# Kernel optimization log

Hardware: AMD Instinct MI355X
Metric: run time of the kernel (lower is better)

## Reference

```python
import jax, jax.numpy as jnp
import numpy as np

WINDOW, STRIDE, BLUR_THR, EPS = 8, 4, 50.0, 1e-5
DN = ('NCHW', 'OIHW', 'NCHW')


def _conv(x, w, pad=0, stride=1):
    return jax.lax.conv_general_dilated(x, w, (stride, stride), [(pad, pad), (pad, pad)], dimension_numbers=DN)


def _detect_rgb_invalid(rgb):
    # Laplacian-variance blur detector: unfold(8,stride=4) -> var -> threshold -> scatter windows
    B, _, H, W = rgb.shape
    gray = 0.299 * rgb[:, 0] + 0.587 * rgb[:, 1] + 0.114 * rgb[:, 2]
    gray = jnp.clip(gray * 255.0, 0.0, 255.0)[:, None]  # [B,1,H,W]
    lap_k = jnp.array([[0., 1., 0.], [1., -4., 1.], [0., 1., 0.]], gray.dtype)[None, None]
    lap = _conv(gray, lap_k, pad=1)
    ones_k = jnp.ones((1, 1, WINDOW, WINDOW), gray.dtype)
    s1 = jax.lax.conv_general_dilated(lap, ones_k, (STRIDE, STRIDE), 'VALID', dimension_numbers=DN)
    s2 = jax.lax.conv_general_dilated(lap * lap, ones_k, (STRIDE, STRIDE), 'VALID', dimension_numbers=DN)
    n = float(WINDOW * WINDOW)
    var = (s2 - s1 * s1 / n) / (n - 1.0)  # unbiased var, matches torch.var
    flags = (var[:, 0] < BLUR_THR).astype(gray.dtype)  # [B, hs, ws]
    hs, ws = flags.shape[1], flags.shape[2]
    rep = jnp.repeat(jnp.repeat(flags, STRIDE, axis=1), STRIDE, axis=2)  # [B, hs*4, ws*4]
    mask = jnp.zeros((B, H, W), gray.dtype)
    # each 8x8 window covers 2x2 stride-cells -> max over the 4 shifted copies
    for dy in range(0, WINDOW, STRIDE):
        for dx in range(0, WINDOW, STRIDE):
            mask = mask.at[:, dy:dy + hs * STRIDE, dx:dx + ws * STRIDE].max(rep)
    return mask


def _bn_relu(x, g, b):
    m = x.mean((0, 2, 3), keepdims=True)
    v = x.var((0, 2, 3), keepdims=True)  # biased, matches BN training-mode normalization
    return jax.nn.relu(g[None, :, None, None] * (x - m) / jnp.sqrt(v + EPS) + b[None, :, None, None])


def _attend(main, aux, inv, ft_w, bn_g, bn_b, sa_w, ca1_w, ca2_w):
    B, C, H, W = main.shape
    aux_t = _bn_relu(_conv(aux, ft_w, pad=1), bn_g, bn_b)
    xs = jnp.broadcast_to(jnp.linspace(-1.0, 1.0, W, dtype=main.dtype)[None, None, None, :], (B, 1, H, W))
    ys = jnp.broadcast_to(jnp.linspace(-1.0, 1.0, H, dtype=main.dtype)[None, None, :, None], (B, 1, H, W))
    sp_in = jnp.concatenate([main.mean(1, keepdims=True), main.max(axis=1, keepdims=True), xs, ys], axis=1)
    sw = jax.nn.sigmoid(_conv(sp_in, sa_w, pad=3))  # [B,1,H,W]
    gap = main.mean((2, 3), keepdims=True)
    cw = jax.nn.sigmoid(_conv(jax.nn.relu(_conv(gap, ca1_w)), ca2_w))  # [B,C,1,1]
    return aux_t * sw * cw * (1.0 + inv[:, None])


def _compensate(main, aux, inv, params):
    # early-return when mask is all-zero in torch is mathematically identical to the blend
    comp = _attend(main, aux, inv, *params)
    m = inv[:, None]
    return main * (1.0 - m) + comp * m


def _down(mask, h, w):
    H, W = mask.shape[1], mask.shape[2]
    return mask[:, ::H // h, ::W // w]  # exact nearest-neighbor for integer ratios


def _forward(rgb_feat0, rgb_feat1, rgb_feat2, depth_feat0, depth_feat1, depth_feat2, rgb_img, depth_img,
             ft_w0, bn_g0, bn_b0, sa_w0, ca1_w0, ca2_w0,
             ft_w1, bn_g1, bn_b1, sa_w1, ca1_w1, ca2_w1,
             ft_w2, bn_g2, bn_b2, sa_w2, ca1_w2, ca2_w2):
    rgb_mask = _detect_rgb_invalid(rgb_img)
    depth_mask = (depth_img[:, 2] <= 0.0).astype(rgb_img.dtype)
    rgb_feats = (rgb_feat0, rgb_feat1, rgb_feat2)
    depth_feats = (depth_feat0, depth_feat1, depth_feat2)
    params = ((ft_w0, bn_g0, bn_b0, sa_w0, ca1_w0, ca2_w0),
              (ft_w1, bn_g1, bn_b1, sa_w1, ca1_w1, ca2_w1),
              (ft_w2, bn_g2, bn_b2, sa_w2, ca1_w2, ca2_w2))
    outs_r, outs_d = [], []
    for rf, df, p in zip(rgb_feats, depth_feats, params):
        h, w = rf.shape[2], rf.shape[3]
        ri = _down(rgb_mask, h, w)
        di = _down(depth_mask, h, w)
        outs_r.append(_compensate(rf, df, ri, p))
        outs_d.append(_compensate(df, rf, di, p))
    return tuple(outs_r) + tuple(outs_d)


def setup_inputs() -> dict:
    key = jax.random.key(0)
    ks = iter(jax.random.split(key, 40))
    B, H, W = 8, 512, 512
    chans = [256, 512, 1024]
    feat_hw = [(64, 64), (32, 32), (16, 16)]
    d = {}
    for i, (C, (fh, fw)) in enumerate(zip(chans, feat_hw)):
        d[f'rgb_feat{i}'] = jax.random.normal(next(ks), (B, C, fh, fw), jnp.float32)
        d[f'depth_feat{i}'] = jax.random.normal(next(ks), (B, C, fh, fw), jnp.float32)
    d['rgb_img'] = jax.random.uniform(next(ks), (B, 3, H, W), jnp.float32)
    d['depth_img'] = jax.random.normal(next(ks), (B, 3, H, W), jnp.float32)
    for i, C in enumerate(chans):
        r = C // 16
        d[f'ft_w{i}'] = jax.random.normal(next(ks), (C, C, 3, 3), jnp.float32) * 0.02
        d[f'bn_g{i}'] = jnp.ones((C,), jnp.float32)
        d[f'bn_b{i}'] = jnp.zeros((C,), jnp.float32)
        d[f'sa_w{i}'] = jax.random.normal(next(ks), (1, 4, 7, 7), jnp.float32) * 0.1
        d[f'ca1_w{i}'] = jax.random.normal(next(ks), (r, C, 1, 1), jnp.float32) * 0.1
        d[f'ca2_w{i}'] = jax.random.normal(next(ks), (C, r, 1, 1), jnp.float32) * 0.1
    return d


def reference(rgb_feat0, rgb_feat1, rgb_feat2, depth_feat0, depth_feat1, depth_feat2, rgb_img, depth_img,
              ft_w0, bn_g0, bn_b0, sa_w0, ca1_w0, ca2_w0,
              ft_w1, bn_g1, bn_b1, sa_w1, ca1_w1, ca2_w1,
              ft_w2, bn_g2, bn_b2, sa_w2, ca1_w2, ca2_w2):
    return _forward(rgb_feat0, rgb_feat1, rgb_feat2, depth_feat0, depth_feat1, depth_feat2, rgb_img, depth_img,
                    ft_w0, bn_g0, bn_b0, sa_w0, ca1_w0, ca2_w0,
                    ft_w1, bn_g1, bn_b1, sa_w1, ca1_w1, ca2_w1,
                    ft_w2, bn_g2, bn_b2, sa_w2, ca1_w2, ca2_w2)
```

## Files before the change

kernel.cpp:

```cpp
#include <hip/hip_runtime.h>
#include <math.h>

#define B8 8
typedef unsigned short ushort_t;
typedef __attribute__((ext_vector_type(8))) short bf16x8;
typedef __attribute__((ext_vector_type(4))) float f32x4;

static __device__ __forceinline__ float sigmoidf_(float x){ return 1.f/(1.f+expf(-x)); }

static __device__ __forceinline__ ushort_t f2bf(float f){
  unsigned u = __float_as_uint(f);
  u = u + 0x7fffu + ((u>>16)&1u);
  return (ushort_t)(u>>16);
}
static __device__ __forceinline__ float bflo(unsigned q){ return __uint_as_float(q << 16); }
static __device__ __forceinline__ float bfhi(unsigned q){ return __uint_as_float(q & 0xffff0000u); }

__device__ __forceinline__ void gload_lds16(const ushort_t* g, ushort_t* l){
  __builtin_amdgcn_global_load_lds((const __attribute__((address_space(1))) unsigned int*)(const void*)g,
                                   (__attribute__((address_space(3))) unsigned int*)(void*)l, 16, 0, 0);
}

__global__ __launch_bounds__(256) void k_flags2(const float* __restrict__ rgb,
                                                float* __restrict__ flags){
  __shared__ float sg[70][71];
  int bx = blockIdx.x & 7, by = (blockIdx.x >> 3) & 7, b = blockIdx.x >> 6;
  int wy0 = by*16, wx0 = bx*16;
  int y0 = 4*wy0 - 1, x0 = 4*wx0 - 1;
  const float* p = rgb + (size_t)b*3*262144;
  int tid = threadIdx.x;
  for (int i = tid; i < 70*70; i += 256){
    int r = i/70, cX = i%70;
    int y = y0 + r, x = x0 + cX;
    float v = 0.f;
    if (y>=0 && y<512 && x>=0 && x<512){
      int ii = y*512+x;
      v = 0.299f*p[ii] + 0.587f*p[ii+262144] + 0.114f*p[ii+524288];
      v = fminf(fmaxf(v*255.f, 0.f), 255.f);
    }
    sg[r][cX] = v;
  }
  __syncthreads();
  int wy = wy0 + (tid>>4), wx = wx0 + (tid&15);
  if (wy > 126 || wx > 126) return;
  int ry = 4*(tid>>4) + 1, rx = 4*(tid&15) + 1;
  float s1 = 0.f, s2 = 0.f;
  #pragma unroll
  for (int iy=0; iy<8; ++iy){
    int r = ry+iy;
    #pragma unroll
    for (int ix=0; ix<8; ++ix){
      int cX = rx+ix;
      float c = sg[r][cX];
      float lap = sg[r-1][cX] + sg[r+1][cX] + sg[r][cX-1] + sg[r][cX+1] - 4.f*c;
      s1 += lap; s2 += lap*lap;
    }
  }
  float var = (s2 - s1*s1*(1.f/64.f)) * (1.f/63.f);
  flags[(size_t)b*16129 + wy*127 + wx] = (var < 50.f) ? 1.f : 0.f;
}

__global__ void k_masks3(const float* __restrict__ flags, const float* __restrict__ depth,
                         float* __restrict__ ri0, float* __restrict__ di0,
                         float* __restrict__ ri1, float* __restrict__ di1,
                         float* __restrict__ ri2, float* __restrict__ di2){
  int idx = blockIdx.x*256 + threadIdx.x;
  const int n0 = 8*4096, n1 = 8*1024, n2 = 8*256;
  float* ri; float* di; int h, st, i2;
  if (idx < n0){ ri=ri0; di=di0; h=64; st=8;  i2=idx; }
  else if (idx < n0+n1){ ri=ri1; di=di1; h=32; st=16; i2=idx-n0; }
  else if (idx < n0+n1+n2){ ri=ri2; di=di2; h=16; st=32; i2=idx-n0-n1; }
  else return;
  int b = i2/(h*h), i = i2%(h*h);
  int y = (i/h)*st, x = (i%h)*st;
  const float* f = flags + (size_t)b*16129;
  int fy = y>>2, fx = x>>2;
  float v = f[fy*127+fx];
  if (y>0)         v = fmaxf(v, f[(fy-1)*127+fx]);
  if (x>0)         v = fmaxf(v, f[fy*127+fx-1]);
  if (y>0 && x>0)  v = fmaxf(v, f[(fy-1)*127+fx-1]);
  ri[i2] = v;
  const int IHW = 262144;
  di[i2] = (depth[(size_t)b*3*IHW + 2*IHW + (size_t)y*512 + x] <= 0.f) ? 1.f : 0.f;
}

template<int C>
__global__ __launch_bounds__(256) void k_wrd2(const float* __restrict__ w, ushort_t* __restrict__ outp){
  __shared__ float swp[9*C];
  int co = blockIdx.x, tid = threadIdx.x;
  const int n = 9*C;
  const float* src = w + (size_t)co*n;
  for (int i=tid;i<n;i+=256) swp[i]=src[i];
  __syncthreads();
  ushort_t* dst = outp + (size_t)co*n;
  for (int j=tid;j<n;j+=256){
    int cb  = j / 576;
    int rem = j - cb*576;
    int kq  = rem >> 6;
    int cin = rem & 63;
    dst[j] = f2bf(swp[(cb*64 + cin)*9 + kq]);
  }
}

template<int C, int H, int W>
__global__ __launch_bounds__(256) void k_nhwc2(const float* __restrict__ rgbf,
                                               const float* __restrict__ depf,
                                               ushort_t* __restrict__ outp){
  const int W2 = W+2, H2 = H+2, CB = C/64;
  const int NHSZ = B8*H2*W2*C;
  __shared__ float st[64*66];
  int bi = blockIdx.x;
  int dir = bi & 1; bi >>= 1;
  int cb  = bi % CB; bi /= CB;
  int yy  = bi % H2;
  int b   = bi / H2;
  int tid = threadIdx.x;
  const float* in = (dir==0) ? depf : rgbf;
  ushort_t* outrow = outp + (size_t)dir*NHSZ + ((size_t)(b*H2 + yy)*W2)*C + cb*64;
  bool pad_row = (yy == 0) || (yy == H2-1);
  if (!pad_row){
    int y = yy-1;
    const float* src = in + ((size_t)(b*C + cb*64)*H + y)*W;
    for (int i=tid; i<64*W; i+=256){
      int c = i / W, x = i % W;
      st[x*66 + c] = src[(size_t)c*H*W + x];
    }
  }
  __syncthreads();
  for (int j=tid; j<W2*8; j+=256){
    int x = j >> 3, cc = (j & 7)*8;
    ushort_t tmp[8];
    if (pad_row || x == 0 || x == W2-1){
      #pragma unroll
      for (int q=0;q<8;++q) tmp[q]=0;
    } else {
      const float* sp = &st[(x-1)*66 + cc];
      float2 a0 = *(const float2*)(sp+0);
      float2 a1 = *(const float2*)(sp+2);
      float2 a2 = *(const float2*)(sp+4);
      float2 a3 = *(const float2*)(sp+6);
      tmp[0]=f2bf(a0.x); tmp[1]=f2bf(a0.y); tmp[2]=f2bf(a1.x); tmp[3]=f2bf(a1.y);
      tmp[4]=f2bf(a2.x); tmp[5]=f2bf(a2.y); tmp[6]=f2bf(a3.x); tmp[7]=f2bf(a3.y);
    }
    *(bf16x8*)&outrow[(size_t)x*C + cc] = *(bf16x8*)tmp;
  }
}

template<int C, int H, int W, int KS>
__global__ __launch_bounds__(512)
void k_gemm_conv(const ushort_t* __restrict__ Aw, const ushort_t* __restrict__ nh,
                 ushort_t* __restrict__ Gm){
  const int K9 = 9*C;
  const int HW = H*W;
  const int N  = B8*HW;
  const int H2 = H+2, W2 = W+2;
  const int NT_N = N/256, NT_M = C/256;
  const int KCT = 36;
  const int NHSZ = B8*H2*W2*C;
  __shared__ ushort_t sA[2][16384];
  __shared__ ushort_t sB[2][16384];
  int tid = threadIdx.x;

  const int nwg = 2*KS*NT_M*NT_N;
  const int MK  = 2*KS*NT_M;
  int bid = blockIdx.x;
  int swz = (bid & 7)*(nwg >> 3) + (bid >> 3);
  int mk  = swz % MK;
  int n_t = swz / MK;
  int m_t = mk % NT_M;
  int kz2 = mk / NT_M;
  int dir = kz2 / KS, kz = kz2 % KS;

  const ushort_t* nhd = nh + (size_t)dir*NHSZ;
  int m0 = m_t*256, n0 = n_t*256;
  int l = tid & 63, wv_id = tid >> 6;
  int wm = wv_id >> 2, wn = wv_id & 3;
  int lrow = l & 15, lq = l >> 4;
  int lx7 = lrow & 7;

  long long aoffA[2][2], boffB[2][2];
  #pragma unroll
  for (int h=0; h<2; ++h){
    #pragma unroll
    for (int j=0; j<2; ++j){
      int c = j*512 + tid;
      int lr = h*128 + (c>>3);
      int slot = c & 7;
      int lslot = slot ^ (lr & 7);
      int q_ = lr >> 6, wm_ = (lr>>5)&1, loc = lr & 31;
      int r = wm_*128 + q_*32 + loc;
      aoffA[h][j] = (long long)(m0 + r)*K9 + lslot*8;
      int nn = n0 + lr;
      int b_ = nn / HW, rhw = nn % HW;
      int y = rhw / W, x = rhw % W;
      boffB[h][j] = ((long long)(b_*H2 + y + 1)*W2 + (x + 1))*(long long)C + lslot*8;
    }
  }

#define STAGE_A(s_, h_, kc_) do{                                    \
    long long oK = (long long)(kc_) << 6;                           \
    ushort_t* d0 = &sA[s_][(h_)*8192 + tid*8];                      \
    gload_lds16(Aw + aoffA[h_][0] + oK, d0);                        \
    gload_lds16(Aw + aoffA[h_][1] + oK, d0 + 4096);                 \
  }while(0)
#define STAGE_B(s_, h_, kc_) do{                                    \
    int cb_ = (kc_)/9, kq_ = (kc_) - cb_*9;                         \
    long long dv = (long long)((kq_/3 - 1)*W2 + (kq_%3 - 1))*C + ((long long)cb_<<6); \
    ushort_t* d0 = &sB[s_][(h_)*8192 + tid*8];                      \
    gload_lds16(nhd + boffB[h_][0] + dv, d0);                       \
    gload_lds16(nhd + boffB[h_][1] + dv, d0 + 4096);                \
  }while(0)

  f32x4 acc[8][4];
  #pragma unroll
  for (int i=0;i<8;++i)
    #pragma unroll
    for (int j=0;j<4;++j) acc[i][j] = (f32x4){0.f,0.f,0.f,0.f};

  int kc0 = kz*KCT;

  STAGE_A(0,0,kc0);   STAGE_A(0,1,kc0);
  STAGE_B(0,0,kc0);   STAGE_B(0,1,kc0);
  STAGE_B(1,0,kc0+1); STAGE_B(1,1,kc0+1);
  STAGE_A(1,0,kc0+1);
  asm volatile("s_waitcnt vmcnt(6)" ::: "memory");
  __builtin_amdgcn_s_barrier();

  for (int t=0; t<KCT; ++t){
    int cur = t & 1, nxt = cur ^ 1;
    int kc = kc0 + t;
    bf16x8 bf[4][2], afA[2][2], afB[2][2];

    #pragma unroll
    for (int ni=0;ni<4;++ni)
      #pragma unroll
      for (int kk=0;kk<2;++kk)
        bf[ni][kk] = *(const bf16x8*)&sB[cur][(wn*64 + ni*16 + lrow)*64 + ((kk*4+lq)^lx7)*8];
    #pragma unroll
    for (int mi=0;mi<2;++mi)
      #pragma unroll
      for (int kk=0;kk<2;++kk)
        afA[mi][kk] = *(const bf16x8*)&sA[cur][(wm*32 + mi*16 + lrow)*64 + ((kk*4+lq)^lx7)*8];
    #pragma unroll
    for (int mi=0;mi<2;++mi)
      #pragma unroll
      for (int kk=0;kk<2;++kk)
        afB[mi][kk] = *(const bf16x8*)&sA[cur][(64 + wm*32 + mi*16 + lrow)*64 + ((kk*4+lq)^lx7)*8];
    if (t+1 < KCT) STAGE_A(nxt,1,kc+1);
    __builtin_amdgcn_s_setprio(1);
    #pragma unroll
    for (int kk=0;kk<2;++kk)
      #pragma unroll
      for (int mi=0;mi<2;++mi)
        #pragma unroll
        for (int ni=0;ni<4;++ni)
          acc[mi][ni] = __builtin_amdgcn_mfma_f32_16x16x32_bf16(afA[mi][kk], bf[ni][kk], acc[mi][ni], 0,0,0);
    __builtin_amdgcn_s_setprio(0);
    asm volatile("s_waitcnt lgkmcnt(0)" ::: "memory");
    __builtin_amdgcn_sched_barrier(0);
    __builtin_amdgcn_s_barrier();

    #pragma unroll
    for (int mi=0;mi<2;++mi)
      #pragma unroll
      for (int kk=0;kk<2;++kk)
        afA[mi][kk] = *(const bf16x8*)&sA[cur][(128 + wm*32 + mi*16 + lrow)*64 + ((kk*4+lq)^lx7)*8];
    if (t+2 < KCT) STAGE_B(cur,0,kc+2);
    __builtin_amdgcn_s_setprio(1);
    #pragma unroll
    for (int kk=0;kk<2;++kk)
      #pragma unroll
      for (int mi=0;mi<2;++mi)
        #pragma unroll
        for (int ni=0;ni<4;++ni)
          acc[2+mi][ni] = __builtin_amdgcn_mfma_f32_16x16x32_bf16(afB[mi][kk], bf[ni][kk], acc[2+mi][ni], 0,0,0);
    __builtin_amdgcn_s_setprio(0);

    #pragma unroll
    for (int mi=0;mi<2;++mi)
      #pragma unroll
      for (int kk=0;kk<2;++kk)
        afB[mi][kk] = *(const bf16x8*)&sA[cur][(192 + wm*32 + mi*16 + lrow)*64 + ((kk*4+lq)^lx7)*8];
    if (t+2 < KCT) STAGE_B(cur,1,kc+2);
    __builtin_amdgcn_s_setprio(1);
    #pragma unroll
    for (int kk=0;kk<2;++kk)
      #pragma unroll
      for (int mi=0;mi<2;++mi)
        #pragma unroll
        for (int ni=0;ni<4;++ni)
          acc[4+mi][ni] = __builtin_amdgcn_mfma_f32_16x16x32_bf16(afA[mi][kk], bf[ni][kk], acc[4+mi][ni], 0,0,0);
    __builtin_amdgcn_s_setprio(0);

    if (t+2 < KCT) STAGE_A(cur,0,kc+2);
    __builtin_amdgcn_s_setprio(1);
    #pragma unroll
    for (int kk=0;kk<2;++kk)
      #pragma unroll
      for (int mi=0;mi<2;++mi)
        #pragma unroll
        for (int ni=0;ni<4;++ni)
          acc[6+mi][ni] = __builtin_amdgcn_mfma_f32_16x16x32_bf16(afB[mi][kk], bf[ni][kk], acc[6+mi][ni], 0,0,0);
    __builtin_amdgcn_s_setprio(0);
    if (t+2 < KCT) { asm volatile("s_waitcnt vmcnt(6)" ::: "memory"); }
    else           { asm volatile("s_waitcnt vmcnt(0)" ::: "memory"); }
    __builtin_amdgcn_sched_barrier(0);
    __builtin_amdgcn_s_barrier();
  }
#undef STAGE_A
#undef STAGE_B

  ushort_t* po = Gm + (size_t)kz2*C*N;
  #pragma unroll
  for (int ai=0;ai<8;++ai)
    #pragma unroll
    for (int ni=0;ni<4;++ni)
      #pragma unroll
      for (int r=0;r<4;++r)
        po[(size_t)(m0 + wm*128 + ai*16 + lq*4 + r)*N + n0 + wn*64 + ni*16 + lrow] = f2bf(acc[ai][ni][r]);
}

template<int C, int HW, int SPLIT>
__global__ __launch_bounds__(256) void k_sg(const float* __restrict__ rgbf,
                                            const float* __restrict__ depf,
                                            float* __restrict__ gpart,
                                            float* __restrict__ pmean,
                                            float* __restrict__ pmax_){
  const int CG = C/32;
  const int POS = HW/SPLIT;
  int dir = blockIdx.y;
  const float* main_ = (dir==0) ? rgbf : depf;
  int bi = blockIdx.x;
  int sp = bi % SPLIT; bi /= SPLIT;
  int cg = bi % CG;    int b = bi / CG;
  const float* base = main_ + ((size_t)b*C + (size_t)cg*32)*HW + (size_t)sp*POS;
  int tid = threadIdx.x;
  float csum[32];
  #pragma unroll
  for (int c=0;c<32;++c) csum[c]=0.f;
  size_t po = ((size_t)dir*CG + cg)*((size_t)B8*HW) + (size_t)b*HW + (size_t)sp*POS;

  if constexpr (POS >= 1024){
    const int P4 = POS/4;
    for (int p = tid; p < P4; p += 256){
      float4 ps = {0.f,0.f,0.f,0.f};
      float4 pm = {-INFINITY,-INFINITY,-INFINITY,-INFINITY};
      #pragma unroll
      for (int c=0;c<32;++c){
        float4 v = *(const float4*)(base + (size_t)c*HW + (size_t)p*4);
        csum[c] += v.x+v.y+v.z+v.w;
        ps.x+=v.x; ps.y+=v.y; ps.z+=v.z; ps.w+=v.w;
        pm.x=fmaxf(pm.x,v.x); pm.y=fmaxf(pm.y,v.y); pm.z=fmaxf(pm.z,v.z); pm.w=fmaxf(pm.w,v.w);
      }
      *(float4*)(pmean + po + (size_t)p*4) = ps;
      *(float4*)(pmax_ + po + (size_t)p*4) = pm;
    }
  } else {
    int p = tid;
    if (p < POS){
      float ps = 0.f, pm = -INFINITY;
      #pragma unroll
      for (int c=0;c<32;++c){
        float v = base[(size_t)c*HW + p];
        csum[c] += v;
        ps += v; pm = fmaxf(pm, v);
      }
      pmean[po + p] = ps;
      pmax_[po + p] = pm;
    }
  }
  __shared__ float red[4][32];
  int lane = tid & 63, w = tid >> 6;
  #pragma unroll
  for (int c=0;c<32;++c){
    float s = csum[c];
    #pragma unroll
    for (int off=32; off; off>>=1) s += __shfl_down(s, off);
    if (lane == 0) red[w][c] = s;
  }
  __syncthreads();
  if (tid < 32){
    float s = red[0][tid]+red[1][tid]+red[2][tid]+red[3][tid];
    gpart[(((size_t)dir*B8 + b)*SPLIT + sp)*C + (size_t)cg*32 + tid] = s;
  }
}

__global__ void k_sgc(const float* __restrict__ pmean, const float* __restrict__ pmax_,
                      float* __restrict__ spmean, float* __restrict__ spmax,
                      int CG, int BHW, float invC){
  int dir = blockIdx.y;
  int p = blockIdx.x*256 + threadIdx.x;
  if (p >= BHW) return;
  const float* pm = pmean + (size_t)dir*CG*BHW;
  const float* px = pmax_ + (size_t)dir*CG*BHW;
  float s = 0.f, m = -INFINITY;
  for (int g=0; g<CG; ++g){
    s += pm[(size_t)g*BHW + p];
    m = fmaxf(m, px[(size_t)g*BHW + p]);
  }
  spmean[(size_t)dir*BHW + p] = s*invC;
  spmax [(size_t)dir*BHW + p] = m;
}

__global__ void k_sw(const float* __restrict__ spmean, const float* __restrict__ spmax,
                     const float* __restrict__ sa, float* __restrict__ sw,
                     int H, int W){
  __shared__ float s_sa[196];
  int tid = threadIdx.x;
  if (tid < 196) s_sa[tid] = sa[tid];
  __syncthreads();
  int HW = H*W;
  int dir = blockIdx.y;
  int gpos = blockIdx.x*256 + tid;
  if (gpos >= B8*HW) return;
  int b = gpos/HW, i = gpos%HW;
  int y = i/W, x = i%W;
  float inv_w = 2.f/(float)(W-1), inv_h = 2.f/(float)(H-1);
  const float* pm = spmean + (size_t)dir*B8*HW + (size_t)b*HW;
  const float* px = spmax  + (size_t)dir*B8*HW + (size_t)b*HW;
  float acc = 0.f;
  for (int ky=0;ky<7;++ky){
    int yy = y+ky-3;
    if (yy<0 || yy>=H) continue;
    float ysv = -1.f + yy*inv_h;
    for (int kx=0;kx<7;++kx){
      int xx = x+kx-3;
      if (xx<0 || xx>=W) continue;
      float xsv = -1.f + xx*inv_w;
      int kk = ky*7+kx;
      acc += s_sa[kk]*pm[yy*W+xx] + s_sa[49+kk]*px[yy*W+xx]
           + s_sa[98+kk]*xsv + s_sa[147+kk]*ysv;
    }
  }
  sw[(size_t)dir*B8*HW + gpos] = sigmoidf_(acc);
}

__global__ void k_mlp(const float* __restrict__ gpart, const float* __restrict__ w1,
                      const float* __restrict__ w2, float* __restrict__ cw,
                      int C, int R, int SPLIT, float invHW){
  int b = blockIdx.x, dir = blockIdx.y;
  int tid = threadIdx.x;
  __shared__ float sg[1024];
  __shared__ float sh[64];
  const float* gp = gpart + (((size_t)dir*B8 + b)*SPLIT)*C;
  for (int c=tid;c<C;c+=256){
    float s = 0.f;
    for (int sp=0; sp<SPLIT; ++sp) s += gp[(size_t)sp*C + c];
    sg[c] = s*invHW;
  }
  __syncthreads();
  int r = tid>>2, q = tid&3;
  if (r < R){
    float s = 0.f;
    for (int c=q;c<C;c+=4) s += w1[(size_t)r*C + c]*sg[c];
    s += __shfl_xor(s,1); s += __shfl_xor(s,2);
    if (q==0) sh[r] = fmaxf(s, 0.f);
  }
  __syncthreads();
  for (int c2=tid; c2<C; c2+=256){
    float s = 0.f;
    for (int rr=0;rr<R;++rr) s += w2[(size_t)c2*R + rr]*sh[rr];
    cw[(size_t)dir*B8*C + (size_t)b*C + c2] = sigmoidf_(s);
  }
}

__global__ __launch_bounds__(256)
void k_bnfinal(const float* __restrict__ rgbf, const float* __restrict__ depf,
               const ushort_t* __restrict__ G,
               const float* __restrict__ g, const float* __restrict__ bb,
               const float* __restrict__ swp, const float* __restrict__ cwp,
               const float* __restrict__ ri, const float* __restrict__ di,
               float* __restrict__ out_r, float* __restrict__ out_d,
               int C, int HW, int hwShift, int ks){
  extern __shared__ char bnf_smem[];
  int c = blockIdx.x, dir = blockIdx.y, tid = threadIdx.x;
  int N = B8*HW;
  size_t MN = (size_t)C*N;
  const ushort_t* p0 = G + (size_t)dir*ks*MN + (size_t)c*N;
  const float* main_ = (dir==0) ? rgbf : depf;
  const float* mask  = (dir==0) ? ri : di;
  float* out = (dir==0) ? out_r : out_d;

  float s1 = 0.f, s2 = 0.f;
  if (ks == 1){
    uint4* cache = (uint4*)bnf_smem;
    for (int i = tid*8; i < N; i += 2048){
      uint4 q = *(const uint4*)(p0 + i);
      cache[i>>3] = q;
      float v0=bflo(q.x), v1=bfhi(q.x), v2=bflo(q.y), v3=bfhi(q.y);
      float v4=bflo(q.z), v5=bfhi(q.z), v6=bflo(q.w), v7=bfhi(q.w);
      s1 += v0+v1+v2+v3+v4+v5+v6+v7;
      s2 += v0*v0+v1*v1+v2*v2+v3*v3+v4*v4+v5*v5+v6*v6+v7*v7;
    }
  } else {
    float* cache = (float*)bnf_smem;
    for (int i = tid*8; i < N; i += 2048){
      float v[8];
      #pragma unroll
      for (int q=0;q<8;++q) v[q]=0.f;
      for (int kz=0; kz<ks; ++kz){
        uint4 q = *(const uint4*)(p0 + (size_t)kz*MN + i);
        v[0]+=bflo(q.x); v[1]+=bfhi(q.x); v[2]+=bflo(q.y); v[3]+=bfhi(q.y);
        v[4]+=bflo(q.z); v[5]+=bfhi(q.z); v[6]+=bflo(q.w); v[7]+=bfhi(q.w);
      }
      #pragma unroll
      for (int q=0;q<8;++q){ cache[i+q] = v[q]; s1 += v[q]; s2 += v[q]*v[q]; }
    }
  }
  __shared__ float sb1[4], sb2[4];
  __shared__ float sab[2];
  #pragma unroll
  for (int off=32; off; off>>=1){ s1 += __shfl_down(s1,off); s2 += __shfl_down(s2,off); }
  int wid = tid>>6;
  if ((tid&63)==0){ sb1[wid]=s1; sb2[wid]=s2; }
  __syncthreads();
  if (tid==0){
    float t1 = sb1[0]+sb1[1]+sb1[2]+sb1[3];
    float t2 = sb2[0]+sb2[1]+sb2[2]+sb2[3];
    float Nf = (float)N;
    float mean = t1/Nf;
    float var  = t2/Nf - mean*mean;
    float a = g[c] / sqrtf(var + 1e-5f);
    sab[0] = a;
    sab[1] = bb[c] - mean*a;
  }
  __syncthreads();
  float a = sab[0], bta = sab[1];

  for (int i = tid*8; i < N; i += 2048){
    float v[8];
    if (ks == 1){
      uint4 q = ((const uint4*)bnf_smem)[i>>3];
      v[0]=bflo(q.x); v[1]=bfhi(q.x); v[2]=bflo(q.y); v[3]=bfhi(q.y);
      v[4]=bflo(q.z); v[5]=bfhi(q.z); v[6]=bflo(q.w); v[7]=bfhi(q.w);
    } else {
      #pragma unroll
      for (int q=0;q<8;++q) v[q] = ((const float*)bnf_smem)[i+q];
    }
    int b  = i >> hwShift;
    int hw = i - (b << hwShift);
    const float* mkp = mask + (size_t)b*HW + hw;
    const float* mnp = main_ + ((size_t)b*C + c)*HW + hw;
    const float* swq = swp + (size_t)dir*B8*HW + (size_t)b*HW + hw;
    float cwv = 2.f * cwp[(size_t)dir*B8*C + (size_t)b*C + c];
    float4 mk0 = *(const float4*)(mkp),   mk1 = *(const float4*)(mkp+4);
    float4 mn0 = *(const float4*)(mnp),   mn1 = *(const float4*)(mnp+4);
    float4 sw0 = *(const float4*)(swq),   sw1 = *(const float4*)(swq+4);
    float4 o0, o1;
    o0.x = (mk0.x > 0.5f) ? fmaxf(a*v[0] + bta, 0.f)*sw0.x*cwv : mn0.x;
    o0.y = (mk0.y > 0.5f) ? fmaxf(a*v[1] + bta, 0.f)*sw0.y*cwv : mn0.y;
    o0.z = (mk0.z > 0.5f) ? fmaxf(a*v[2] + bta, 0.f)*sw0.z*cwv : mn0.z;
    o0.w = (mk0.w > 0.5f) ? fmaxf(a*v[3] + bta, 0.f)*sw0.w*cwv : mn0.w;
    o1.x = (mk1.x > 0.5f) ? fmaxf(a*v[4] + bta, 0.f)*sw1.x*cwv : mn1.x;
    o1.y = (mk1.y > 0.5f) ? fmaxf(a*v[5] + bta, 0.f)*sw1.y*cwv : mn1.y;
    o1.z = (mk1.z > 0.5f) ? fmaxf(a*v[6] + bta, 0.f)*sw1.z*cwv : mn1.z;
    o1.w = (mk1.w > 0.5f) ? fmaxf(a*v[7] + bta, 0.f)*sw1.w*cwv : mn1.w;
    float* op = out + ((size_t)b*C + c)*HW + hw;
    *(float4*)(op)   = o0;
    *(float4*)(op+4) = o1;
  }
}

extern "C" void kernel_launch(void* const* d_in, const int* in_sizes, int n_in,
                              void* d_out, int out_size, void* d_ws, size_t ws_size,
                              hipStream_t stream){
  (void)in_sizes; (void)n_in; (void)out_size; (void)ws_size;
  const int B = B8;
  const float* rgb_feat[3] = {(const float*)d_in[0], (const float*)d_in[2], (const float*)d_in[4]};
  const float* dep_feat[3] = {(const float*)d_in[1], (const float*)d_in[3], (const float*)d_in[5]};
  const float* rgb_img = (const float*)d_in[6];
  const float* dep_img = (const float*)d_in[7];

  const int Cs[3]   = {256, 512, 1024};
  const int hs[3]   = {64, 32, 16};
  const int HWs[3]  = {64*64, 32*32, 16*16};
  const int KSs[3]  = {1, 2, 4};
  const int SPL[3]  = {4, 1, 1};
  const int HWSH[3] = {12, 10, 8};
  const unsigned BNSM[3] = {65536, 32768, 8192};

  float* ws = (float*)d_ws;
  ushort_t* Gm = (ushort_t*)ws;
  float* flags = ws;
  float* rdbase = ws + 8388608;
  float* ri[3]; float* di[3];
  {
    size_t o = 0;
    for (int s=0;s<3;++s){
      ri[s] = rdbase + o; o += (size_t)B*hs[s]*hs[s];
      di[s] = rdbase + o; o += (size_t)B*hs[s]*hs[s];
    }
  }
  float* SB = rdbase + 86016;

  float* swb    = SB + 0;
  float* gpart  = SB + 65536;
  float* cwb    = SB + 81920;
  float* spmean = SB + 98304;
  float* spmax  = SB + 163840;
  float* pmeanp = SB + 229376;
  float* pmaxp  = SB + 753664;

  k_flags2<<<512, 256, 0, stream>>>(rgb_img, flags);
  k_masks3<<<168, 256, 0, stream>>>(flags, dep_img, ri[0], di[0], ri[1], di[1], ri[2], di[2]);

  const size_t outoff_r[3] = {0,         8388608u,  12582912u};
  const size_t outoff_d[3] = {14680064u, 23068672u, 27262976u};
  float* outp = (float*)d_out;

  for (int s=0;s<3;++s){
    const float* ftw = (const float*)d_in[8 +6*s];
    const float* bng = (const float*)d_in[9 +6*s];
    const float* bnb = (const float*)d_in[10+6*s];
    const float* saw = (const float*)d_in[11+6*s];
    const float* ca1 = (const float*)d_in[12+6*s];
    const float* ca2 = (const float*)d_in[13+6*s];
    int C = Cs[s], HW = HWs[s], h = hs[s];
    int R = C/16;
    int BHW = B*HW;
    int ks = KSs[s];

    size_t nh_f = (size_t)B*(h+2)*(h+2)*C;
    ushort_t* nhbf = (ushort_t*)SB;
    ushort_t* wbf  = (ushort_t*)(SB + nh_f);

    if (s==0) k_wrd2<256> <<<256,  256, 0, stream>>>(ftw, wbf);
    if (s==1) k_wrd2<512> <<<512,  256, 0, stream>>>(ftw, wbf);
    if (s==2) k_wrd2<1024><<<1024, 256, 0, stream>>>(ftw, wbf);

    {
      unsigned nb = (unsigned)(B*(h+2)*(C/64)*2);
      if (s==0) k_nhwc2<256, 64,64><<<nb, 256, 0, stream>>>(rgb_feat[s], dep_feat[s], nhbf);
      if (s==1) k_nhwc2<512, 32,32><<<nb, 256, 0, stream>>>(rgb_feat[s], dep_feat[s], nhbf);
      if (s==2) k_nhwc2<1024,16,16><<<nb, 256, 0, stream>>>(rgb_feat[s], dep_feat[s], nhbf);
    }

    if (s==0) k_gemm_conv<256, 64,64,1><<<256, 512, 0, stream>>>(wbf, nhbf, Gm);
    if (s==1) k_gemm_conv<512, 32,32,2><<<256, 512, 0, stream>>>(wbf, nhbf, Gm);
    if (s==2) k_gemm_conv<1024,16,16,4><<<256, 512, 0, stream>>>(wbf, nhbf, Gm);

    {
      if (s==0) k_sg<256, 4096, 4><<<dim3((unsigned)(B*(256/32)*4),2),  256, 0, stream>>>(rgb_feat[s], dep_feat[s], gpart, pmeanp, pmaxp);
      if (s==1) k_sg<512, 1024, 1><<<dim3((unsigned)(B*(512/32)),2),    256, 0, stream>>>(rgb_feat[s], dep_feat[s], gpart, pmeanp, pmaxp);
      if (s==2) k_sg<1024, 256, 1><<<dim3((unsigned)(B*(1024/32)),2),   256, 0, stream>>>(rgb_feat[s], dep_feat[s], gpart, pmeanp, pmaxp);
      k_sgc<<<dim3((BHW+255)/256,2), 256, 0, stream>>>(pmeanp, pmaxp, spmean, spmax, C/32, BHW, 1.f/(float)C);
    }

    k_sw <<<dim3((B*HW+255)/256,2), 256, 0, stream>>>(spmean, spmax, saw, swb, h, h);
    k_mlp<<<dim3(B,2), 256, 0, stream>>>(gpart, ca1, ca2, cwb, C, R, SPL[s], 1.f/(float)HW);

    k_bnfinal<<<dim3(C,2), 256, BNSM[s], stream>>>(
        rgb_feat[s], dep_feat[s], Gm, bng, bnb, swb, cwb,
        ri[s], di[s], outp + outoff_r[s], outp + outoff_d[s], C, HW, HWSH[s], ks);
  }
}
```

Before: 560.3 us.

## Fuse spatial/channel pooling statistics into the NHWC bf16 repack kernel

```diff
diff --git a/kernel.cpp b/kernel.cpp
--- a/kernel.cpp
+++ b/kernel.cpp
@@ -103,20 +103,26 @@
 }
 
 template<int C, int H, int W>
-__global__ __launch_bounds__(256) void k_nhwc2(const float* __restrict__ rgbf,
-                                               const float* __restrict__ depf,
-                                               ushort_t* __restrict__ outp){
+__global__ __launch_bounds__(256) void k_prep(const float* __restrict__ rgbf,
+                                              const float* __restrict__ depf,
+                                              ushort_t* __restrict__ outp,
+                                              float* __restrict__ gpart,
+                                              float* __restrict__ pmean,
+                                              float* __restrict__ pmax_){
   const int W2 = W+2, H2 = H+2, CB = C/64;
   const int NHSZ = B8*H2*W2*C;
+  const int HW = H*W;
   __shared__ float st[64*66];
+  __shared__ float red[4][64];
   int bi = blockIdx.x;
-  int dir = bi & 1; bi >>= 1;
-  int cb  = bi % CB; bi /= CB;
-  int yy  = bi % H2;
-  int b   = bi / H2;
+  int f  = bi & 1; bi >>= 1;
+  int cb = bi % CB; bi /= CB;
+  int yy = bi % H2;
+  int b  = bi / H2;
   int tid = threadIdx.x;
-  const float* in = (dir==0) ? depf : rgbf;
-  ushort_t* outrow = outp + (size_t)dir*NHSZ + ((size_t)(b*H2 + yy)*W2)*C + cb*64;
+  const float* in = (f==0) ? rgbf : depf;
+  int ndir = f ^ 1;
+  ushort_t* outrow = outp + (size_t)ndir*NHSZ + ((size_t)(b*H2 + yy)*W2)*C + cb*64;
   bool pad_row = (yy == 0) || (yy == H2-1);
   if (!pad_row){
     int y = yy-1;
@@ -143,6 +149,34 @@
       tmp[4]=f2bf(a2.x); tmp[5]=f2bf(a2.y); tmp[6]=f2bf(a3.x); tmp[7]=f2bf(a3.y);
     }
     *(bf16x8*)&outrow[(size_t)x*C + cc] = *(bf16x8*)tmp;
+  }
+  if (pad_row) return;
+  int y = yy - 1;
+  {
+    int c = tid & 63, quarter = tid >> 6;
+    float s = 0.f;
+    for (int x = quarter; x < W; x += 4) s += st[x*66 + c];
+    red[quarter][c] = s;
+  }
+  if (tid < W*4){
+    int x = tid >> 2, sl = tid & 3;
+    float ps = 0.f, pmx = -INFINITY;
+    #pragma unroll
+    for (int k=0;k<16;++k){
+      float v = st[x*66 + sl*16 + k];
+      ps += v; pmx = fmaxf(pmx, v);
+    }
+    ps += __shfl_xor(ps, 1); pmx = fmaxf(pmx, __shfl_xor(pmx, 1));
+    ps += __shfl_xor(ps, 2); pmx = fmaxf(pmx, __shfl_xor(pmx, 2));
+    if (sl == 0){
+      size_t po = ((size_t)f*CB + cb)*((size_t)B8*HW) + (size_t)b*HW + (size_t)y*W + x;
+      pmean[po] = ps; pmax_[po] = pmx;
+    }
+  }
+  __syncthreads();
+  if (tid < 64){
+    float t4 = red[0][tid]+red[1][tid]+red[2][tid]+red[3][tid];
+    gpart[(((size_t)f*B8 + b)*H + y)*C + (size_t)cb*64 + tid] = t4;
   }
 }
 
@@ -318,71 +352,6 @@
       #pragma unroll
       for (int r=0;r<4;++r)
         po[(size_t)(m0 + wm*128 + ai*16 + lq*4 + r)*N + n0 + wn*64 + ni*16 + lrow] = f2bf(acc[ai][ni][r]);
-}
-
-template<int C, int HW, int SPLIT>
-__global__ __launch_bounds__(256) void k_sg(const float* __restrict__ rgbf,
-                                            const float* __restrict__ depf,
-                                            float* __restrict__ gpart,
-                                            float* __restrict__ pmean,
-                                            float* __restrict__ pmax_){
-  const int CG = C/32;
-  const int POS = HW/SPLIT;
-  int dir = blockIdx.y;
-  const float* main_ = (dir==0) ? rgbf : depf;
-  int bi = blockIdx.x;
-  int sp = bi % SPLIT; bi /= SPLIT;
-  int cg = bi % CG;    int b = bi / CG;
-  const float* base = main_ + ((size_t)b*C + (size_t)cg*32)*HW + (size_t)sp*POS;
-  int tid = threadIdx.x;
-  float csum[32];
-  #pragma unroll
-  for (int c=0;c<32;++c) csum[c]=0.f;
-  size_t po = ((size_t)dir*CG + cg)*((size_t)B8*HW) + (size_t)b*HW + (size_t)sp*POS;
-
-  if constexpr (POS >= 1024){
-    const int P4 = POS/4;
-    for (int p = tid; p < P4; p += 256){
-      float4 ps = {0.f,0.f,0.f,0.f};
-      float4 pm = {-INFINITY,-INFINITY,-INFINITY,-INFINITY};
-      #pragma unroll
-      for (int c=0;c<32;++c){
-        float4 v = *(const float4*)(base + (size_t)c*HW + (size_t)p*4);
-        csum[c] += v.x+v.y+v.z+v.w;
-        ps.x+=v.x; ps.y+=v.y; ps.z+=v.z; ps.w+=v.w;
-        pm.x=fmaxf(pm.x,v.x); pm.y=fmaxf(pm.y,v.y); pm.z=fmaxf(pm.z,v.z); pm.w=fmaxf(pm.w,v.w);
-      }
-      *(float4*)(pmean + po + (size_t)p*4) = ps;
-      *(float4*)(pmax_ + po + (size_t)p*4) = pm;
-    }
-  } else {
-    int p = tid;
-    if (p < POS){
-      float ps = 0.f, pm = -INFINITY;
-      #pragma unroll
-      for (int c=0;c<32;++c){
-        float v = base[(size_t)c*HW + p];
-        csum[c] += v;
-        ps += v; pm = fmaxf(pm, v);
-      }
-      pmean[po + p] = ps;
-      pmax_[po + p] = pm;
-    }
-  }
-  __shared__ float red[4][32];
-  int lane = tid & 63, w = tid >> 6;
-  #pragma unroll
-  for (int c=0;c<32;++c){
-    float s = csum[c];
-    #pragma unroll
-    for (int off=32; off; off>>=1) s += __shfl_down(s, off);
-    if (lane == 0) red[w][c] = s;
-  }
-  __syncthreads();
-  if (tid < 32){
-    float s = red[0][tid]+red[1][tid]+red[2][tid]+red[3][tid];
-    gpart[(((size_t)dir*B8 + b)*SPLIT + sp)*C + (size_t)cg*32 + tid] = s;
-  }
 }
 
 __global__ void k_sgc(const float* __restrict__ pmean, const float* __restrict__ pmax_,
@@ -575,7 +544,6 @@
   const int hs[3]   = {64, 32, 16};
   const int HWs[3]  = {64*64, 32*32, 16*16};
   const int KSs[3]  = {1, 2, 4};
-  const int SPL[3]  = {4, 1, 1};
   const int HWSH[3] = {12, 10, 8};
   const unsigned BNSM[3] = {65536, 32768, 8192};
 
@@ -592,14 +560,14 @@
     }
   }
   float* SB = rdbase + 86016;
-
-  float* swb    = SB + 0;
-  float* gpart  = SB + 65536;
-  float* cwb    = SB + 81920;
-  float* spmean = SB + 98304;
-  float* spmax  = SB + 163840;
-  float* pmeanp = SB + 229376;
-  float* pmaxp  = SB + 753664;
+  float* ST = SB + 9220096;
+  float* swb    = ST + 0;
+  float* gpart  = ST + 65536;
+  float* cwb    = ST + 327680;
+  float* spmean = ST + 344064;
+  float* spmax  = ST + 409600;
+  float* pmeanp = ST + 475136;
+  float* pmaxp  = ST + 737280;
 
   k_flags2<<<512, 256, 0, stream>>>(rgb_img, flags);
   k_masks3<<<168, 256, 0, stream>>>(flags, dep_img, ri[0], di[0], ri[1], di[1], ri[2], di[2]);
@@ -630,24 +598,18 @@
 
     {
       unsigned nb = (unsigned)(B*(h+2)*(C/64)*2);
-      if (s==0) k_nhwc2<256, 64,64><<<nb, 256, 0, stream>>>(rgb_feat[s], dep_feat[s], nhbf);
-      if (s==1) k_nhwc2<512, 32,32><<<nb, 256, 0, stream>>>(rgb_feat[s], dep_feat[s], nhbf);
-      if (s==2) k_nhwc2<1024,16,16><<<nb, 256, 0, stream>>>(rgb_feat[s], dep_feat[s], nhbf);
+      if (s==0) k_prep<256, 64,64><<<nb, 256, 0, stream>>>(rgb_feat[s], dep_feat[s], nhbf, gpart, pmeanp, pmaxp);
+      if (s==1) k_prep<512, 32,32><<<nb, 256, 0, stream>>>(rgb_feat[s], dep_feat[s], nhbf, gpart, pmeanp, pmaxp);
+      if (s==2) k_prep<1024,16,16><<<nb, 256, 0, stream>>>(rgb_feat[s], dep_feat[s], nhbf, gpart, pmeanp, pmaxp);
     }
 
     if (s==0) k_gemm_conv<256, 64,64,1><<<256, 512, 0, stream>>>(wbf, nhbf, Gm);
     if (s==1) k_gemm_conv<512, 32,32,2><<<256, 512, 0, stream>>>(wbf, nhbf, Gm);
     if (s==2) k_gemm_conv<1024,16,16,4><<<256, 512, 0, stream>>>(wbf, nhbf, Gm);
 
-    {
-      if (s==0) k_sg<256, 4096, 4><<<dim3((unsigned)(B*(256/32)*4),2),  256, 0, stream>>>(rgb_feat[s], dep_feat[s], gpart, pmeanp, pmaxp);
-      if (s==1) k_sg<512, 1024, 1><<<dim3((unsigned)(B*(512/32)),2),    256, 0, stream>>>(rgb_feat[s], dep_feat[s], gpart, pmeanp, pmaxp);
-      if (s==2) k_sg<1024, 256, 1><<<dim3((unsigned)(B*(1024/32)),2),   256, 0, stream>>>(rgb_feat[s], dep_feat[s], gpart, pmeanp, pmaxp);
-      k_sgc<<<dim3((BHW+255)/256,2), 256, 0, stream>>>(pmeanp, pmaxp, spmean, spmax, C/32, BHW, 1.f/(float)C);
-    }
-
+    k_sgc<<<dim3((BHW+255)/256,2), 256, 0, stream>>>(pmeanp, pmaxp, spmean, spmax, C/64, BHW, 1.f/(float)C);
     k_sw <<<dim3((B*HW+255)/256,2), 256, 0, stream>>>(spmean, spmax, saw, swb, h, h);
-    k_mlp<<<dim3(B,2), 256, 0, stream>>>(gpart, ca1, ca2, cwb, C, R, SPL[s], 1.f/(float)HW);
+    k_mlp<<<dim3(B,2), 256, 0, stream>>>(gpart, ca1, ca2, cwb, C, R, hs[s], 1.f/(float)HW);
 
     k_bnfinal<<<dim3(C,2), 256, BNSM[s], stream>>>(
         rgb_feat[s], dep_feat[s], Gm, bng, bnb, swb, cwb,
```

Result: faster. 518.8 us (-7.4%).
